# Kernel optimization log

Measured on AMD Instinct MI355X. Metric: run time of the kernel, lower is better.

The kernel has to match this reference:

```python
import jax, jax.numpy as jnp
import numpy as np

N, B, E, D, DQ, H = 20000, 32, 320000, 128, 1024, 2
L = N // B  # 625 nodes per graph (equal-size graphs -> static max_node_num)
NUM_GNN_LAYERS = 3


def setup_inputs() -> dict:
    key = jax.random.key(0)
    ks = jax.random.split(key, 32)
    rn = lambda k, s, scale=1.0: jax.random.normal(k, s, jnp.float32) * scale
    w = lambda k, fi, fo: rn(k, (fi, fo), 1.0 / np.sqrt(fi))
    inp = {
        'x': rn(ks[0], (N, D)),
        'edge_attr': rn(ks[1], (E, D)),
        'u': rn(ks[2], (B, D)),
        'qa_attr': rn(ks[3], (B, DQ)),
        # edge MLP: cat(src,dest,edge_attr,u[eb]) = 4D -> hidden D -> D
        'W_e1': w(ks[4], 4 * D, D), 'b_e1': jnp.zeros((D,)),
        'W_e2': w(ks[5], D, D), 'b_e2': jnp.zeros((D,)),
        # weight mlp: cat(edge_attr, u[eb]) = 2D -> 1 (num_layers=1)
        'W_w': w(ks[6], 2 * D, 1), 'b_w': jnp.zeros((1,)),
        # message mlp: cat(x[row], edge_attr) = 2D -> D -> D
        'W_m1': w(ks[7], 2 * D, D), 'b_m1': jnp.zeros((D,)),
        'W_m2': w(ks[8], D, D), 'b_m2': jnp.zeros((D,)),
        # update mlp: cat(x, received, u[nb]) = 3D -> D -> D
        'W_u1': w(ks[9], 3 * D, D), 'b_u1': jnp.zeros((D,)),
        'W_u2': w(ks[10], D, D), 'b_u2': jnp.zeros((D,)),
        # multihead att-pool: q from qa_attr (DQ) -> H*dk; k,v from evidence (D) -> H*dk
        'W_q': w(ks[11], DQ, D), 'b_q': jnp.zeros((D,)),
        'W_k': w(ks[12], D, D), 'b_k': jnp.zeros((D,)),
        'W_v': w(ks[13], D, D), 'b_v': jnp.zeros((D,)),
        'edge_index': jax.random.randint(ks[14], (2, E), 0, N, dtype=jnp.int32),
        'node_batch': (jnp.arange(N, dtype=jnp.int32) // L).astype(jnp.int32),
        'num_of_nodes': jnp.full((B,), L, dtype=jnp.int32),
    }
    return inp


def _mlp2(h, W1, b1, W2, b2):
    return jax.nn.relu(h @ W1 + b1) @ W2 + b2


def _seg_softmax(logits, seg, num):
    m = jax.ops.segment_max(logits, seg, num_segments=num)
    e = jnp.exp(logits - m[seg])
    s = jax.ops.segment_sum(e, seg, num_segments=num)
    return e / s[seg]


def reference(x, edge_attr, u, qa_attr,
              W_e1, b_e1, W_e2, b_e2, W_w, b_w,
              W_m1, b_m1, W_m2, b_m2, W_u1, b_u1, W_u2, b_u2,
              W_q, b_q, W_k, b_k, W_v, b_v,
              edge_index, node_batch, num_of_nodes):
    row, col = edge_index[0], edge_index[1]
    edge_batch = node_batch[row]
    Bsz, Nn = u.shape[0], x.shape[0]
    Lm = Nn // Bsz  # static max_node_num (equal-size graphs)

    norm_w = None
    for _ in range(NUM_GNN_LAYERS):
        ue = u[edge_batch]  # [E, D]
        # EdgeModel: cat(src, dest, edge_attr, u[eb]) -> MLP -> new edge_attr
        new_edge = _mlp2(jnp.concatenate([x[row], x[col], edge_attr, ue], 1),
                         W_e1, b_e1, W_e2, b_e2)
        # edge weights from OLD edge_attr (per EdgeV1Model.forward)
        wts = jnp.concatenate([edge_attr, ue], 1) @ W_w + b_w  # [E,1]
        norm_w = _seg_softmax(wts[:, 0], edge_batch, Bsz)[:, None]  # [E,1]
        edge_attr = new_edge
        # NodeModel: message MLP, weighted scatter_mean over col, update MLP
        msg = _mlp2(jnp.concatenate([x[row], edge_attr], 1), W_m1, b_m1, W_m2, b_m2)
        summed = jax.ops.segment_sum(msg * norm_w, col, num_segments=Nn)
        cnt = jax.ops.segment_sum(jnp.ones((msg.shape[0],), msg.dtype), col, num_segments=Nn)
        received = summed / jnp.maximum(cnt, 1.0)[:, None]
        x = _mlp2(jnp.concatenate([x, received, u[node_batch]], 1),
                  W_u1, b_u1, W_u2, b_u2)

    pooled_edge = jax.ops.segment_sum(edge_attr * norm_w, edge_batch, num_segments=Bsz)  # [B,D]
    # evidence packing: equal graphs -> simple reshape, then exact GELU
    evidence = jax.nn.gelu(x.reshape(Bsz, Lm, -1), approximate=False)  # [B,L,D]
    mask = jnp.arange(Lm)[None, :] >= num_of_nodes[:, None]  # [B,L] True = masked

    # MultiheadAttPoolLayer
    dk = W_k.shape[1] // H
    q = (qa_attr @ W_q + b_q).reshape(Bsz, H, dk)
    k = (evidence @ W_k + b_k).reshape(Bsz, Lm, H, dk)
    v = (evidence @ W_v + b_v).reshape(Bsz, Lm, H, dk)
    scores = jnp.einsum('bhd,blhd->bhl', q, k) / jnp.sqrt(jnp.float32(dk))
    scores = jnp.where(mask[:, None, :], -1e30, scores)
    attn = jax.nn.softmax(scores, axis=-1)
    pooled_node = jnp.einsum('bhl,blhd->bhd', attn, v).reshape(Bsz, H * dk)  # [B,D]

    return jnp.concatenate([pooled_edge, pooled_node], 1)  # [B, 2D]
```

## Files before the change

kernel.cpp:

```cpp
#include <hip/hip_runtime.h>
#include <math.h>

typedef __bf16 bf16_t;
typedef bf16_t bf16x8 __attribute__((ext_vector_type(8)));
typedef bf16_t bf16x4 __attribute__((ext_vector_type(4)));
typedef bf16_t bf16x2 __attribute__((ext_vector_type(2)));
typedef float  f32x4  __attribute__((ext_vector_type(4)));

#define N_NODES 20000
#define NEDGE   320000
#define DIM     128
#define TP      136
#define EBLK    2500
#define FBLK    10000
#define NBLK    625
#define GPRE    157
#define PBLK    512

#define FE1  0
#define FE2  49152
#define FM1  65536
#define FM2  98304
#define FU1  114688
#define FU2  163840
#define FK   180224
#define FV   196608
#define WF_ELEMS 212992

__device__ __forceinline__ void acc_zero32(f32x4 acc[2][8]) {
  f32x4 z = {0.f, 0.f, 0.f, 0.f};
#pragma unroll
  for (int i = 0; i < 2; ++i)
#pragma unroll
    for (int j = 0; j < 8; ++j) acc[i][j] = z;
}

__device__ __forceinline__ void wstage_rows_bf(bf16_t* sA, const bf16_t* src, int rowreg, int lane) {
  int r = lane >> 1, h = lane & 1;
  int row = __shfl(rowreg, r);
  const bf16_t* sp = src + (size_t)row * DIM + h * 64;
  bf16_t* dp = sA + r * TP + h * 64;
#pragma unroll
  for (int i = 0; i < 8; ++i)
    *(uint4*)(dp + i * 8) = *(const uint4*)(sp + i * 8);
}

__device__ __forceinline__ void wstage_rows_f32(bf16_t* sA, const float* src, int rowreg, int lane) {
  int r = lane >> 1, h = lane & 1;
  int row = __shfl(rowreg, r);
  const float* sp = src + (size_t)row * DIM + h * 64;
  bf16_t* dp = sA + r * TP + h * 64;
#pragma unroll
  for (int i = 0; i < 8; ++i) {
    float4 f0 = *(const float4*)(sp + i * 8);
    float4 f1 = *(const float4*)(sp + i * 8 + 4);
    bf16x8 tv;
    tv[0]=(bf16_t)f0.x; tv[1]=(bf16_t)f0.y; tv[2]=(bf16_t)f0.z; tv[3]=(bf16_t)f0.w;
    tv[4]=(bf16_t)f1.x; tv[5]=(bf16_t)f1.y; tv[6]=(bf16_t)f1.z; tv[7]=(bf16_t)f1.w;
    *(bf16x8*)(dp + i * 8) = tv;
  }
}

__device__ __forceinline__ void wstage_seq_bf(bf16_t* sA, const bf16_t* src, int base, int lane) {
  int r = lane >> 1, h = lane & 1;
  const bf16_t* sp = src + (size_t)(base + r) * DIM + h * 64;
  bf16_t* dp = sA + r * TP + h * 64;
#pragma unroll
  for (int i = 0; i < 8; ++i)
    *(uint4*)(dp + i * 8) = *(const uint4*)(sp + i * 8);
}

__device__ __forceinline__ void wstage_seq_f32(bf16_t* sA, const float* src, int base, int lane) {
  int r = lane >> 1, h = lane & 1;
  const float* sp = src + (size_t)(base + r) * DIM + h * 64;
  bf16_t* dp = sA + r * TP + h * 64;
#pragma unroll
  for (int i = 0; i < 8; ++i) {
    float4 f0 = *(const float4*)(sp + i * 8);
    float4 f1 = *(const float4*)(sp + i * 8 + 4);
    bf16x8 tv;
    tv[0]=(bf16_t)f0.x; tv[1]=(bf16_t)f0.y; tv[2]=(bf16_t)f0.z; tv[3]=(bf16_t)f0.w;
    tv[4]=(bf16_t)f1.x; tv[5]=(bf16_t)f1.y; tv[6]=(bf16_t)f1.z; tv[7]=(bf16_t)f1.w;
    *(bf16x8*)(dp + i * 8) = tv;
  }
}

__device__ __forceinline__ void chunk_stage(bf16_t* ch, const bf16_t* __restrict__ src, int t) {
#pragma unroll
  for (int i = 0; i < 8; ++i) {
    int idx = (i * 256 + t) * 8;
    *(uint4*)(ch + idx) = *(const uint4*)(src + idx);
  }
}

__device__ __forceinline__ void wmfma_lds(const bf16_t* sA, const bf16_t* ch,
                                          int lane, int lm, int lq, f32x4 acc[2][8]) {
#pragma unroll
  for (int kk = 0; kk < 4; ++kk) {
    int ko = kk * 32 + lq * 8;
    bf16x8 a0 = *(const bf16x8*)(sA + lm * TP + ko);
    bf16x8 a1 = *(const bf16x8*)(sA + (16 + lm) * TP + ko);
    const bf16_t* wp = ch + (kk << 12) + (lane << 3);
#pragma unroll
    for (int ct = 0; ct < 8; ++ct) {
      bf16x8 bfr = *(const bf16x8*)(wp + (ct << 9));
      acc[0][ct] = __builtin_amdgcn_mfma_f32_16x16x32_bf16(a0, bfr, acc[0][ct], 0, 0, 0);
      acc[1][ct] = __builtin_amdgcn_mfma_f32_16x16x32_bf16(a1, bfr, acc[1][ct], 0, 0, 0);
    }
  }
}

__device__ __forceinline__ void wmfma_gk128(const bf16_t* sA, const bf16_t* __restrict__ Wf,
                                            int lane, int lm, int lq, f32x4 acc[2][8]) {
#pragma unroll
  for (int kk = 0; kk < 4; ++kk) {
    int ko = kk * 32 + lq * 8;
    bf16x8 a0 = *(const bf16x8*)(sA + lm * TP + ko);
    bf16x8 a1 = *(const bf16x8*)(sA + (16 + lm) * TP + ko);
    const bf16_t* wp = Wf + ((kk * 8) << 9) + (lane << 3);
#pragma unroll
    for (int ct = 0; ct < 8; ++ct) {
      bf16x8 bfr = *(const bf16x8*)(wp + (ct << 9));
      acc[0][ct] = __builtin_amdgcn_mfma_f32_16x16x32_bf16(a0, bfr, acc[0][ct], 0, 0, 0);
      acc[1][ct] = __builtin_amdgcn_mfma_f32_16x16x32_bf16(a1, bfr, acc[1][ct], 0, 0, 0);
    }
  }
}

__device__ __forceinline__ void merge_shfl(float& m, float& s, int width) {
  for (int k = 1; k < width; k <<= 1) {
    float m2 = __shfl_xor(m, k), s2 = __shfl_xor(s, k);
    float M = fmaxf(m, m2), ns = 0.f;
    if (m  > -1e29f) ns += s  * expf(m  - M);
    if (m2 > -1e29f) ns += s2 * expf(m2 - M);
    m = M; s = ns;
  }
}

__global__ void gn_xcvt(const float* x, bf16_t* xb) {
  int i = blockIdx.x * 256 + threadIdx.x;
  if (i < N_NODES * DIM / 4) {
    float4 f = ((const float4*)x)[i];
    bf16x4 o; o[0]=(bf16_t)f.x; o[1]=(bf16_t)f.y; o[2]=(bf16_t)f.z; o[3]=(bf16_t)f.w;
    *(bf16x4*)(xb + (size_t)i * 4) = o;
  }
}

__global__ void gn_fragw(const float* We1, const float* We2, const float* Wm1, const float* Wm2,
                         const float* Wu1, const float* Wu2, const float* Wk, const float* Wv,
                         bf16_t* WF) {
  int idx = blockIdx.x * 256 + threadIdx.x;
  if (idx >= WF_ELEMS) return;
  int seg = idx >> 14;
  const float* W; int kc;
  switch (seg) {
    case 0:  W = We1; kc = 0; break;
    case 1:  W = We1; kc = 1; break;
    case 2:  W = We1; kc = 2; break;
    case 3:  W = We2; kc = 0; break;
    case 4:  W = Wm1; kc = 0; break;
    case 5:  W = Wm1; kc = 1; break;
    case 6:  W = Wm2; kc = 0; break;
    case 7:  W = Wu1; kc = 0; break;
    case 8:  W = Wu1; kc = 1; break;
    case 9:  W = Wu1; kc = 2; break;
    case 10: W = Wu2; kc = 0; break;
    case 11: W = Wk;  kc = 0; break;
    default: W = Wv;  kc = 0; break;
  }
  int r = idx & 16383;
  int j = r & 7, lane = (r >> 3) & 63, ct = (r >> 9) & 7, kk = (r >> 12) & 3;
  int k = kc * 128 + kk * 32 + (lane >> 4) * 8 + j;
  int n = ct * 16 + (lane & 15);
  WF[idx] = (bf16_t)W[k * 128 + n];
}

__global__ void gn_uprep(const float* u, const float* We1, const float* be1,
                         const float* Ww, const float* bw, float* Rp, float* uw) {
  int t = threadIdx.x;
  for (int idx = blockIdx.x * 256 + t; idx < 32 * 128; idx += gridDim.x * 256) {
    int g = idx >> 7, c = idx & 127;
    float acc = be1[c];
    for (int k = 0; k < 128; ++k) acc += u[g * 128 + k] * We1[(384 + k) * 128 + c];
    Rp[g * 128 + (c & 15) * 8 + (c >> 4)] = acc;
  }
  if (blockIdx.x == 0 && t < 32) {
    float acc = bw[0];
    for (int k = 0; k < 128; ++k) acc += u[t * 128 + k] * Ww[128 + k];
    uw[t] = acc;
  }
}

__global__ void gn_counti(const int* ei, int* cnti) {
  int e = blockIdx.x * 256 + threadIdx.x;
  if (e < NEDGE) atomicAdd(&cnti[ei[NEDGE + e]], 1);
}

__global__ void gn_scan(const int* cnti, int* off, int* curs) {
  __shared__ int part[256];
  int t = threadIdx.x;
  int base = t * 80;
  int lim = base + 80; if (lim > N_NODES) lim = N_NODES;
  int s = 0;
  for (int i = base; i < lim; ++i) s += cnti[i];
  part[t] = s;
  __syncthreads();
  for (int d = 1; d < 256; d <<= 1) {
    int add = (t >= d) ? part[t - d] : 0;
    __syncthreads();
    part[t] += add;
    __syncthreads();
  }
  int pfx = (t == 0) ? 0 : part[t - 1];
  for (int i = base; i < lim; ++i) {
    off[i] = pfx; curs[i] = pfx; pfx += cnti[i];
  }
  if (t == 0) off[N_NODES] = NEDGE;
}

__global__ void gn_eidx(const int* ei, int* curs, int* eidx) {
  int e = blockIdx.x * 256 + threadIdx.x;
  if (e < NEDGE) {
    int c = ei[NEDGE + e];
    int pos = atomicAdd(&curs[c], 1);
    eidx[pos] = e;
  }
}

__global__ void gn_q(const float* qa, const float* Wq, const float* bq, float* qb) {
  int b = blockIdx.x, t = threadIdx.x;
  int c = t & 127, half = t >> 7;
  const float* qrow = qa + b * 1024 + half * 512;
  float acc = 0.f;
  for (int k = 0; k < 512; ++k) acc += qrow[k] * Wq[(half * 512 + k) * 128 + c];
  __shared__ float red[256];
  red[t] = acc;
  __syncthreads();
  if (half == 0) qb[b * 128 + c] = red[c] + red[128 + c] + bq[c];
}

__global__ void gn_wl0(const float* ea, const float* Ww, const float* uw,
                       const int* ei, const int* nbat, float* wl, int* gb) {
  int t = threadIdx.x;
  int sub = t & 15, grp = t >> 4;
  for (int e = blockIdx.x * 16 + grp; e < NEDGE; e += gridDim.x * 16) {
    const float* er = ea + (size_t)e * DIM + sub * 8;
    float s = 0.f;
#pragma unroll
    for (int j = 0; j < 8; ++j) s += er[j] * Ww[sub * 8 + j];
#pragma unroll
    for (int m = 1; m < 16; m <<= 1) s += __shfl_xor(s, m);
    if (sub == 0) {
      int g = nbat[ei[e]];
      wl[e] = s + uw[g];
      gb[e] = g;
    }
  }
}

__global__ void gn_part0(const float* wl, const int* gb, float* pm, float* ps) {
  __shared__ float lv[128];
  __shared__ int   lgg[128];
  int t = threadIdx.x, blk = blockIdx.x, e0 = blk * 128;
  if (t < 128) { lv[t] = wl[e0 + t]; lgg[t] = gb[e0 + t]; }
  __syncthreads();
  int g = t >> 3, seg = t & 7;
  float m = -1e30f, s = 0.f;
  for (int i = seg * 16; i < seg * 16 + 16; ++i)
    if (lgg[i] == g) {
      float v = lv[i];
      if (v > m) { s = s * expf(m - v) + 1.f; m = v; }
      else s += expf(v - m);
    }
  merge_shfl(m, s, 8);
  if (seg == 0) { pm[blk * 32 + g] = m; ps[blk * 32 + g] = s; }
}

__global__ void gn_reduce_ms(const float* pm, const float* ps, float* mg, float* sg, int nb) {
  int g = blockIdx.x, t = threadIdx.x;
  __shared__ float red[256];
  float m = -1e30f;
  for (int i = t; i < nb; i += 256) m = fmaxf(m, pm[i * 32 + g]);
  red[t] = m; __syncthreads();
  for (int s2 = 128; s2 > 0; s2 >>= 1) { if (t < s2) red[t] = fmaxf(red[t], red[t + s2]); __syncthreads(); }
  m = red[0]; __syncthreads();
  float s = 0.f;
  for (int i = t; i < nb; i += 256) {
    float sb = ps[i * 32 + g];
    if (sb > 0.f) s += sb * expf(pm[i * 32 + g] - m);
  }
  red[t] = s; __syncthreads();
  for (int s2 = 128; s2 > 0; s2 >>= 1) { if (t < s2) red[t] += red[t + s2]; __syncthreads(); }
  if (t == 0) { mg[g] = m; sg[g] = red[0]; }
}

__global__ __launch_bounds__(256, 2) void gn_fused(
    const bf16_t* __restrict__ xb,
    const void* esrcv, int efirst,
    bf16_t* edst,
    const bf16_t* __restrict__ WF,
    const float* Rp, const float* UW, const float* Wwv,
    const float* be2, const float* bm1, const float* bm2,
    const float* wl_cur, const float* mg, const float* sg,
    float* wl_next, float* pm, float* ps, int last,
    const int* ei, const int* gb, bf16_t* msg,
    const float* uu, const float* bu1, const int* nbat, float* pre,
    float* nwout) {
  __shared__ bf16_t chunk[16384];
  __shared__ bf16_t band[4][32 * TP];
  __shared__ float slwt[128];

  int t = threadIdx.x;
  int w = t >> 6, lane = t & 63;
  int lm = lane & 15, lq = lane >> 4;
  int blk = blockIdx.x;
  bf16_t* myband = band[w];

  if (blk >= EBLK) {
    int nb128 = blk - EBLK;
    int gb32 = nb128 * 4 + w;
    int lrow = 0, lgr = 0;
    if (lane < 32) {
      int node = gb32 * 32 + lane;
      if (node > N_NODES - 1) node = N_NODES - 1;
      lrow = node;
      lgr = nbat[node];
    }
    f32x4 acc[2][8];
    acc_zero32(acc);
    wstage_rows_bf(myband, xb, lrow, lane);
    chunk_stage(chunk, WF + FU1, t);
    __syncthreads();
    wmfma_lds(myband, chunk, lane, lm, lq, acc);
    __syncthreads();
    wstage_rows_f32(myband, uu, lgr, lane);
    chunk_stage(chunk, WF + FU1 + 32768, t);
    __syncthreads();
    wmfma_lds(myband, chunk, lane, lm, lq, acc);
    if (gb32 < NBLK) {
      float* pp = pre + (size_t)gb32 * 4096 + lane;
#pragma unroll
      for (int rt = 0; rt < 2; ++rt)
#pragma unroll
        for (int reg = 0; reg < 4; ++reg)
#pragma unroll
          for (int ct = 0; ct < 8; ++ct)
            pp[((rt * 32 + reg * 8 + ct) << 6)] = acc[rt][ct][reg] + bu1[ct * 16 + lm];
    }
    return;
  }

  int e0 = blk * 128;
  int ew0 = e0 + w * 32;
  int lrowr = 0, lcolr = 0, lgr = 0;
  float lnwr = 0.f;
  if (lane < 32) {
    int e = ew0 + lane;
    lrowr = ei[e];
    lcolr = ei[NEDGE + e];
    lgr = gb[e];
    lnwr = expf(wl_cur[e] - mg[lgr]) / sg[lgr];
    if (last) nwout[e] = lnwr;
  }

  f32x4 accE[2][8], accM[2][8];
  acc_zero32(accE);
  acc_zero32(accM);

  uint4 c0, c1, c2, c3, c4, c5, c6, c7;
#define CLOAD(SRC) { const uint4* _s = (const uint4*)(SRC) + t; \
  c0 = _s[0];    c1 = _s[256];  c2 = _s[512];  c3 = _s[768]; \
  c4 = _s[1024]; c5 = _s[1280]; c6 = _s[1536]; c7 = _s[1792]; }
#define CWRITE() { uint4* _d = (uint4*)chunk + t; \
  _d[0] = c0;    _d[256] = c1;  _d[512] = c2;  _d[768] = c3; \
  _d[1024] = c4; _d[1280] = c5; _d[1536] = c6; _d[1792] = c7; }

  CLOAD(WF + FE1);
  wstage_rows_bf(myband, xb, lrowr, lane);
  CWRITE();
  __syncthreads();

  CLOAD(WF + FM1);
  wmfma_lds(myband, chunk, lane, lm, lq, accE);
  __syncthreads();
  CWRITE();
  __syncthreads();

  CLOAD(WF + FE1 + 16384);
  wmfma_lds(myband, chunk, lane, lm, lq, accM);
  wstage_rows_bf(myband, xb, lcolr, lane);
  __syncthreads();
  CWRITE();
  __syncthreads();

  CLOAD(WF + FE1 + 32768);
  wmfma_lds(myband, chunk, lane, lm, lq, accE);
  if (efirst) wstage_seq_f32(myband, (const float*)esrcv, ew0, lane);
  else        wstage_seq_bf (myband, (const bf16_t*)esrcv, ew0, lane);
  __syncthreads();
  CWRITE();
  __syncthreads();

  CLOAD(WF + FE2);
  wmfma_lds(myband, chunk, lane, lm, lq, accE);
#pragma unroll
  for (int rt = 0; rt < 2; ++rt)
#pragma unroll
    for (int reg = 0; reg < 4; ++reg) {
      int row = rt * 16 + lq * 4 + reg;
      int g = __shfl(lgr, row);
      const float4* rp = (const float4*)(Rp + (size_t)g * 128 + lm * 8);
      float4 ra = rp[0], rb = rp[1];
      float rv[8] = {ra.x, ra.y, ra.z, ra.w, rb.x, rb.y, rb.z, rb.w};
#pragma unroll
      for (int ct = 0; ct < 8; ++ct) {
        int col = ct * 16 + lm;
        myband[row * TP + col] = (bf16_t)fmaxf(accE[rt][ct][reg] + rv[ct], 0.f);
      }
    }
  acc_zero32(accE);
  __syncthreads();
  CWRITE();
  __syncthreads();

  CLOAD(WF + FM1 + 16384);
  wmfma_lds(myband, chunk, lane, lm, lq, accE);
  {
    float ww8[8], be8[8];
#pragma unroll
    for (int ct = 0; ct < 8; ++ct) { ww8[ct] = Wwv[ct * 16 + lm]; be8[ct] = be2[ct * 16 + lm]; }
#pragma unroll
    for (int rt = 0; rt < 2; ++rt)
#pragma unroll
      for (int reg = 0; reg < 4; ++reg) {
        int row = rt * 16 + lq * 4 + reg;
        int g = __shfl(lgr, row);
        float lsum = 0.f;
#pragma unroll
        for (int ct = 0; ct < 8; ++ct) {
          int col = ct * 16 + lm;
          float v = accE[rt][ct][reg] + be8[ct];
          myband[row * TP + col] = (bf16_t)v;
          lsum += v * ww8[ct];
        }
        if (!last) {
          lsum += __shfl_xor(lsum, 1);
          lsum += __shfl_xor(lsum, 2);
          lsum += __shfl_xor(lsum, 4);
          lsum += __shfl_xor(lsum, 8);
          if (lm == 0) {
            float v2 = lsum + UW[g];
            wl_next[ew0 + row] = v2;
            slwt[w * 32 + row] = v2;
          }
        }
      }
    int r = lane >> 1, h = lane & 1;
    bf16_t* dp = edst + (size_t)(ew0 + r) * DIM + h * 64;
    const bf16_t* sp2 = myband + r * TP + h * 64;
#pragma unroll
    for (int i = 0; i < 8; ++i)
      *(uint4*)(dp + i * 8) = *(const uint4*)(sp2 + i * 8);
  }
  __syncthreads();
  CWRITE();
  __syncthreads();

  CLOAD(WF + FM2);
  wmfma_lds(myband, chunk, lane, lm, lq, accM);
  {
    float bm18[8];
#pragma unroll
    for (int ct = 0; ct < 8; ++ct) bm18[ct] = bm1[ct * 16 + lm];
#pragma unroll
    for (int rt = 0; rt < 2; ++rt)
#pragma unroll
      for (int reg = 0; reg < 4; ++reg) {
        int row = rt * 16 + lq * 4 + reg;
#pragma unroll
        for (int ct = 0; ct < 8; ++ct) {
          int col = ct * 16 + lm;
          myband[row * TP + col] = (bf16_t)fmaxf(accM[rt][ct][reg] + bm18[ct], 0.f);
        }
      }
  }
  acc_zero32(accM);
  __syncthreads();
  CWRITE();
  __syncthreads();

  wmfma_lds(myband, chunk, lane, lm, lq, accM);
  {
    float bm28[8];
#pragma unroll
    for (int ct = 0; ct < 8; ++ct) bm28[ct] = bm2[ct * 16 + lm];
#pragma unroll
    for (int rt = 0; rt < 2; ++rt)
#pragma unroll
      for (int reg = 0; reg < 4; ++reg) {
        int row = rt * 16 + lq * 4 + reg;
        float nwv = __shfl(lnwr, row);
#pragma unroll
        for (int ct = 0; ct < 8; ++ct) {
          int col = ct * 16 + lm;
          myband[row * TP + col] = (bf16_t)((accM[rt][ct][reg] + bm28[ct]) * nwv);
        }
      }
    int r = lane >> 1, h = lane & 1;
    bf16_t* dp = msg + (size_t)(ew0 + r) * DIM + h * 64;
    const bf16_t* sp2 = myband + r * TP + h * 64;
#pragma unroll
    for (int i = 0; i < 8; ++i)
      *(uint4*)(dp + i * 8) = *(const uint4*)(sp2 + i * 8);
  }

  if (!last) {
    int g = lane >> 1, seg = lane & 1;
    float m = -1e30f, s = 0.f;
    for (int i = seg * 16; i < seg * 16 + 16; ++i) {
      int gi = __shfl(lgr, i);
      if (gi == g) {
        float v = slwt[w * 32 + i];
        if (v > m) { s = s * expf(m - v) + 1.f; m = v; }
        else s += expf(v - m);
      }
    }
    merge_shfl(m, s, 2);
    if (seg == 0) { pm[(blk * 4 + w) * 32 + g] = m; ps[(blk * 4 + w) * 32 + g] = s; }
  }
#undef CLOAD
#undef CWRITE
}

__global__ __launch_bounds__(256) void gn_gather(
    const bf16_t* __restrict__ msg, const int* __restrict__ off,
    const int* __restrict__ eidx, bf16_t* recvb) {
  int w = threadIdx.x >> 6, lane = threadIdx.x & 63;
  int n = blockIdx.x * 4 + w;
  int o0 = off[n], o1 = off[n + 1];
  float a0 = 0.f, a1 = 0.f;
  int i = o0;
  int e = (i < o1) ? eidx[i] : 0;
  for (; i < o1; ++i) {
    int en = (i + 1 < o1) ? eidx[i + 1] : 0;
    bf16x2 v = *(const bf16x2*)(msg + (size_t)e * DIM + lane * 2);
    a0 += (float)v[0];
    a1 += (float)v[1];
    e = en;
  }
  float ic = 1.f / fmaxf((float)(o1 - o0), 1.f);
  bf16x2 o; o[0] = (bf16_t)(a0 * ic); o[1] = (bf16_t)(a1 * ic);
  *(bf16x2*)(recvb + (size_t)n * DIM + lane * 2) = o;
}

__global__ __launch_bounds__(64, 3) void gn_node(
    bf16_t* xdst, const bf16_t* recvb, const float* pre,
    const bf16_t* __restrict__ WF, const float* bu2) {
  __shared__ bf16_t sA[32 * TP];

  int lane = threadIdx.x;
  int nb = blockIdx.x;
  int n0 = nb * 32;
  int lm = lane & 15, lq = lane >> 4;

  wstage_seq_bf(sA, recvb, n0, lane);

  f32x4 acc[2][8];
  acc_zero32(acc);
  wmfma_gk128(sA, WF + FU1 + 16384, lane, lm, lq, acc);

  const float* pp = pre + (size_t)nb * 4096 + lane;
#pragma unroll
  for (int rt = 0; rt < 2; ++rt)
#pragma unroll
    for (int reg = 0; reg < 4; ++reg) {
      int row = rt * 16 + lq * 4 + reg;
#pragma unroll
      for (int ct = 0; ct < 8; ++ct) {
        int col = ct * 16 + lm;
        sA[row * TP + col] = (bf16_t)fmaxf(acc[rt][ct][reg] + pp[((rt * 32 + reg * 8 + ct) << 6)], 0.f);
      }
    }
  acc_zero32(acc);
  wmfma_gk128(sA, WF + FU2, lane, lm, lq, acc);

  {
    float bu28[8];
#pragma unroll
    for (int ct = 0; ct < 8; ++ct) bu28[ct] = bu2[ct * 16 + lm];
#pragma unroll
    for (int rt = 0; rt < 2; ++rt)
#pragma unroll
      for (int reg = 0; reg < 4; ++reg) {
        int row = rt * 16 + lq * 4 + reg;
        bf16_t* dr = xdst + (size_t)(n0 + row) * DIM;
#pragma unroll
        for (int ct = 0; ct < 8; ++ct) {
          int col = ct * 16 + lm;
          dr[col] = (bf16_t)(acc[rt][ct][reg] + bu28[ct]);
        }
      }
  }
}

__global__ __launch_bounds__(64, 3) void gn_ev(
    const bf16_t* xsrc, const bf16_t* __restrict__ WF,
    const float* bk, const float* bv, float* kb, float* vb) {
  __shared__ bf16_t sA[32 * TP];

  int lane = threadIdx.x;
  int n0 = blockIdx.x * 32;
  int sel = blockIdx.y;
  const bf16_t* Wf = WF + (sel ? FV : FK);
  const float* bias = sel ? bv : bk;
  float* dst = sel ? vb : kb;
  int lm = lane & 15, lq = lane >> 4;

  {
    int r = lane >> 1, h = lane & 1;
    const bf16_t* sp = xsrc + (size_t)(n0 + r) * DIM + h * 64;
    bf16_t* dp = sA + r * TP + h * 64;
#pragma unroll
    for (int i = 0; i < 8; ++i) {
      uint4 v = *(const uint4*)(sp + i * 8);
      bf16_t tmp[8];
      *(uint4*)tmp = v;
      bf16x8 tv;
#pragma unroll
      for (int j = 0; j < 8; ++j) {
        float f = (float)tmp[j];
        tv[j] = (bf16_t)(0.5f * f * (1.f + erff(f * 0.70710678118654752f)));
      }
      *(bf16x8*)(dp + i * 8) = tv;
    }
  }

  f32x4 acc[2][8];
  acc_zero32(acc);
  wmfma_gk128(sA, Wf, lane, lm, lq, acc);

  {
    float b8[8];
#pragma unroll
    for (int ct = 0; ct < 8; ++ct) b8[ct] = bias[ct * 16 + lm];
#pragma unroll
    for (int rt = 0; rt < 2; ++rt)
#pragma unroll
      for (int reg = 0; reg < 4; ++reg) {
        int row = rt * 16 + lq * 4 + reg;
        float* dr = dst + (size_t)(n0 + row) * DIM;
#pragma unroll
        for (int ct = 0; ct < 8; ++ct) {
          int col = ct * 16 + lm;
          dr[col] = acc[rt][ct][reg] + b8[ct];
        }
      }
  }
}

__global__ __launch_bounds__(256, 2) void gn_pooled_edge(
    const bf16_t* __restrict__ eb, const float* __restrict__ nw,
    const int* __restrict__ gb, float* pep) {
  __shared__ float loc[4][4096];
  int t = threadIdx.x;
  int lane = t & 63, w = t >> 6;
  float* myloc = loc[w];
  for (int i = lane; i < 4096; i += 64) myloc[i] = 0.f;

  int wid = blockIdx.x * 4 + w;
  int c0 = lane * 2;
  for (int e = wid; e < NEDGE; e += PBLK * 4) {
    int g = gb[e];
    float nwt = nw[e];
    bf16x2 v = *(const bf16x2*)(eb + (size_t)e * DIM + c0);
    float* a = myloc + g * 128 + c0;
    float2 cur = *(float2*)a;
    cur.x += (float)v[0] * nwt;
    cur.y += (float)v[1] * nwt;
    *(float2*)a = cur;
  }
  __syncthreads();
  float* pp = pep + (size_t)blockIdx.x * 4096;
  for (int i = t; i < 4096; i += 256)
    pp[i] = loc[0][i] + loc[1][i] + loc[2][i] + loc[3][i];
}

__global__ void gn_att(const float* qb, const float* kb, const float* vb, const int* non, float* out) {
  int b = blockIdx.x >> 1, h = blockIdx.x & 1, t = threadIdx.x;
  __shared__ float qv[64];
  __shared__ float sc[625];
  __shared__ float red[256];
  if (t < 64) qv[t] = qb[b * 128 + h * 64 + t];
  __syncthreads();
  int nn = non[b];
  const float4* qv4 = (const float4*)qv;
  for (int l = t; l < 625; l += 256) {
    float acc = 0.f;
    const float4* kr = (const float4*)(kb + ((size_t)(b * 625 + l)) * DIM + h * 64);
#pragma unroll
    for (int d2 = 0; d2 < 16; ++d2) {
      float4 kv = kr[d2];
      float4 qq = qv4[d2];
      acc += qq.x * kv.x + qq.y * kv.y + qq.z * kv.z + qq.w * kv.w;
    }
    sc[l] = (l < nn) ? acc * 0.125f : -1e30f;
  }
  __syncthreads();
  float m = -1e30f;
  for (int l = t; l < 625; l += 256) m = fmaxf(m, sc[l]);
  red[t] = m; __syncthreads();
  for (int s2 = 128; s2 > 0; s2 >>= 1) { if (t < s2) red[t] = fmaxf(red[t], red[t + s2]); __syncthreads(); }
  m = red[0]; __syncthreads();
  float ssum = 0.f;
  for (int l = t; l < 625; l += 256) { float e = expf(sc[l] - m); sc[l] = e; ssum += e; }
  red[t] = ssum; __syncthreads();
  for (int s2 = 128; s2 > 0; s2 >>= 1) { if (t < s2) red[t] += red[t + s2]; __syncthreads(); }
  float inv = 1.f / red[0];
  __syncthreads();
  int d = t & 63, seg = t >> 6;
  float acc = 0.f;
  for (int l = seg; l < 625; l += 4) acc += sc[l] * vb[((size_t)(b * 625 + l)) * DIM + h * 64 + d];
  red[t] = acc; __syncthreads();
  if (t < 64) {
    float v = red[t] + red[64 + t] + red[128 + t] + red[192 + t];
    out[b * 256 + 128 + h * 64 + d] = v * inv;
  }
}

__global__ void gn_fin(const float* pep, float* out) {
  int i = blockIdx.x * 256 + threadIdx.x;
  float s = 0.f;
#pragma unroll 8
  for (int blk = 0; blk < PBLK; ++blk) s += pep[(size_t)blk * 4096 + i];
  int b = i >> 7, c = i & 127;
  out[b * 256 + c] = s;
}

extern "C" void kernel_launch(void* const* d_in, const int* in_sizes, int n_in,
                              void* d_out, int out_size, void* d_ws, size_t ws_size,
                              hipStream_t stream) {
  const float* x   = (const float*)d_in[0];
  const float* ea  = (const float*)d_in[1];
  const float* u   = (const float*)d_in[2];
  const float* qa  = (const float*)d_in[3];
  const float* We1 = (const float*)d_in[4];
  const float* be1 = (const float*)d_in[5];
  const float* We2 = (const float*)d_in[6];
  const float* be2 = (const float*)d_in[7];
  const float* Ww  = (const float*)d_in[8];
  const float* bw  = (const float*)d_in[9];
  const float* Wm1 = (const float*)d_in[10];
  const float* bm1 = (const float*)d_in[11];
  const float* Wm2 = (const float*)d_in[12];
  const float* bm2 = (const float*)d_in[13];
  const float* Wu1 = (const float*)d_in[14];
  const float* bu1 = (const float*)d_in[15];
  const float* Wu2 = (const float*)d_in[16];
  const float* bu2 = (const float*)d_in[17];
  const float* Wq  = (const float*)d_in[18];
  const float* bq  = (const float*)d_in[19];
  const float* Wk  = (const float*)d_in[20];
  const float* bk  = (const float*)d_in[21];
  const float* Wv  = (const float*)d_in[22];
  const float* bv  = (const float*)d_in[23];
  const int* ei   = (const int*)d_in[24];
  const int* nbat = (const int*)d_in[25];
  const int* non  = (const int*)d_in[26];
  float* out = (float*)d_out;

  char* p = (char*)d_ws;
  auto alloc = [&](size_t bytes) { char* r = p; p += (bytes + 255) & ~(size_t)255; return r; };
  bf16_t* EB    = (bf16_t*)alloc((size_t)NEDGE * DIM * 2);
  bf16_t* XB    = (bf16_t*)alloc((size_t)N_NODES * DIM * 2);
  bf16_t* XB0   = (bf16_t*)alloc((size_t)N_NODES * DIM * 2);
  bf16_t* MSG   = (bf16_t*)alloc((size_t)NEDGE * DIM * 2);
  bf16_t* RECVB = (bf16_t*)alloc((size_t)N_NODES * DIM * 2);
  int*   CNTI = (int*)alloc((size_t)N_NODES * 4);
  int*   OFF  = (int*)alloc((size_t)(N_NODES + 1) * 4);
  int*   CURS = (int*)alloc((size_t)N_NODES * 4);
  int*   EIDX = (int*)alloc((size_t)NEDGE * 4);
  float* WL   = (float*)alloc((size_t)NEDGE * 4);
  float* WLn  = (float*)alloc((size_t)NEDGE * 4);
  float* NW   = (float*)alloc((size_t)NEDGE * 4);
  int*   GB   = (int*)alloc((size_t)NEDGE * 4);
  float* PM   = (float*)alloc((size_t)FBLK * 32 * 4);
  float* PS   = (float*)alloc((size_t)FBLK * 32 * 4);
  float* MG   = (float*)alloc(32 * 4);
  float* SG   = (float*)alloc(32 * 4);
  float* RP   = (float*)alloc(32 * 128 * 4);
  float* UW   = (float*)alloc(32 * 4);
  bf16_t* WF  = (bf16_t*)alloc((size_t)WF_ELEMS * 2);
  float* QB   = (float*)alloc(32 * 128 * 4);
  float* KB   = (float*)alloc((size_t)N_NODES * DIM * 4);
  float* VB   = (float*)alloc((size_t)N_NODES * DIM * 4);
  float* PEP  = (float*)alloc((size_t)PBLK * 4096 * 4);
  float* PRE  = (float*)alloc((size_t)N_NODES * DIM * 4);

  hipMemsetAsync(CNTI, 0, (size_t)N_NODES * 4, stream);

  gn_xcvt<<<(N_NODES * DIM / 4 + 255) / 256, 256, 0, stream>>>(x, XB0);
  gn_fragw<<<(WF_ELEMS + 255) / 256, 256, 0, stream>>>(We1, We2, Wm1, Wm2, Wu1, Wu2, Wk, Wv, WF);
  gn_uprep<<<16, 256, 0, stream>>>(u, We1, be1, Ww, bw, RP, UW);
  gn_counti<<<1250, 256, 0, stream>>>(ei, CNTI);
  gn_scan<<<1, 256, 0, stream>>>(CNTI, OFF, CURS);
  gn_eidx<<<1250, 256, 0, stream>>>(ei, CURS, EIDX);
  gn_q<<<32, 256, 0, stream>>>(qa, Wq, bq, QB);
  gn_wl0<<<2500, 256, 0, stream>>>(ea, Ww, UW, ei, nbat, WL, GB);
  gn_part0<<<EBLK, 256, 0, stream>>>(WL, GB, PM, PS);

  for (int layer = 0; layer < 3; ++layer) {
    int first = (layer == 0) ? 1 : 0;
    int last = (layer == 2) ? 1 : 0;
    const bf16_t* xs = first ? XB0 : XB;
    const void* es = first ? (const void*)ea : (const void*)EB;
    float* cur = (layer == 1) ? WLn : WL;
    float* nxt = (layer == 1) ? WL : WLn;
    gn_reduce_ms<<<32, 256, 0, stream>>>(PM, PS, MG, SG, first ? EBLK : FBLK);
    gn_fused<<<EBLK + GPRE, 256, 0, stream>>>(xs, es, first, EB, WF, RP, UW, Ww,
                                              be2, bm1, bm2, cur, MG, SG,
                                              nxt, PM, PS, last, ei, GB, MSG,
                                              u, bu1, nbat, PRE, NW);
    gn_gather<<<5000, 256, 0, stream>>>(MSG, OFF, EIDX, RECVB);
    gn_node<<<NBLK, 64, 0, stream>>>(XB, RECVB, PRE, WF, bu2);
  }

  gn_pooled_edge<<<PBLK, 256, 0, stream>>>(EB, NW, GB, PEP);
  gn_ev<<<dim3(NBLK, 2), 64, 0, stream>>>(XB, WF, bk, bv, KB, VB);
  gn_att<<<64, 256, 0, stream>>>(QB, KB, VB, non, out);
  gn_fin<<<16, 256, 0, stream>>>(PEP, out);
}
```

Before: 1.334 ms.

## Fold message MLP second layer into update weights via precomputed Wm2·Wu1

Removes the second message-MLP GEMM from the per-edge fused kernel by using linearity. The mean aggregation commutes with the Wm2 projection, so the node kernel multiplies the aggregated hidden activations by a precomputed Wm2·Wu1 block and adds the bias term rnw·(bm2·Wu1). The gather kernel now also averages the per-edge normalized weights to rebuild that bias, and the per-block softmax partials are stored transposed for contiguous reduction reads. This removes one 128x128 GEMM per edge tile plus a weight chunk load, at the cost of always writing nwout and changing bf16 rounding points.

```diff
diff --git a/kernel.cpp b/kernel.cpp
--- a/kernel.cpp
+++ b/kernel.cpp
@@ -12,7 +12,7 @@
 #define DIM     128
 #define TP      136
 #define EBLK    2500
-#define FBLK    10000
+#define FWAVES  10000
 #define NBLK    625
 #define GPRE    157
 #define PBLK    512
@@ -25,7 +25,8 @@
 #define FU2  163840
 #define FK   180224
 #define FV   196608
-#define WF_ELEMS 212992
+#define FWC  212992
+#define WF_ELEMS 229376
 
 __device__ __forceinline__ void acc_zero32(f32x4 acc[2][8]) {
   f32x4 z = {0.f, 0.f, 0.f, 0.f};
@@ -146,9 +147,19 @@
   }
 }
 
+__global__ void gn_wcomb(const float* Wm2, const float* Wu1, float* wc) {
+  int idx = blockIdx.x * 256 + threadIdx.x;
+  if (idx >= 16384) return;
+  int i = idx >> 7, j = idx & 127;
+  float acc = 0.f;
+  for (int m = 0; m < 128; ++m)
+    acc += Wm2[i * 128 + m] * Wu1[(128 + m) * 128 + j];
+  wc[idx] = acc;
+}
+
 __global__ void gn_fragw(const float* We1, const float* We2, const float* Wm1, const float* Wm2,
                          const float* Wu1, const float* Wu2, const float* Wk, const float* Wv,
-                         bf16_t* WF) {
+                         const float* Wc, bf16_t* WF) {
   int idx = blockIdx.x * 256 + threadIdx.x;
   if (idx >= WF_ELEMS) return;
   int seg = idx >> 14;
@@ -166,7 +177,8 @@
     case 9:  W = Wu1; kc = 2; break;
     case 10: W = Wu2; kc = 0; break;
     case 11: W = Wk;  kc = 0; break;
-    default: W = Wv;  kc = 0; break;
+    case 12: W = Wv;  kc = 0; break;
+    default: W = Wc;  kc = 0; break;
   }
   int r = idx & 16383;
   int j = r & 7, lane = (r >> 3) & 63, ct = (r >> 9) & 7, kk = (r >> 12) & 3;
@@ -176,7 +188,9 @@
 }
 
 __global__ void gn_uprep(const float* u, const float* We1, const float* be1,
-                         const float* Ww, const float* bw, float* Rp, float* uw) {
+                         const float* Ww, const float* bw,
+                         const float* bm2, const float* Wu1,
+                         float* Rp, float* uw, float* bm2u) {
   int t = threadIdx.x;
   for (int idx = blockIdx.x * 256 + t; idx < 32 * 128; idx += gridDim.x * 256) {
     int g = idx >> 7, c = idx & 127;
@@ -188,6 +202,11 @@
     float acc = bw[0];
     for (int k = 0; k < 128; ++k) acc += u[t * 128 + k] * Ww[128 + k];
     uw[t] = acc;
+  }
+  if (blockIdx.x == 1 && t < 128) {
+    float acc = 0.f;
+    for (int k = 0; k < 128; ++k) acc += bm2[k] * Wu1[(128 + k) * 128 + t];
+    bm2u[t] = acc;
   }
 }
 
@@ -273,21 +292,21 @@
       else s += expf(v - m);
     }
   merge_shfl(m, s, 8);
-  if (seg == 0) { pm[blk * 32 + g] = m; ps[blk * 32 + g] = s; }
+  if (seg == 0) { pm[g * FWAVES + blk] = m; ps[g * FWAVES + blk] = s; }
 }
 
 __global__ void gn_reduce_ms(const float* pm, const float* ps, float* mg, float* sg, int nb) {
   int g = blockIdx.x, t = threadIdx.x;
   __shared__ float red[256];
   float m = -1e30f;
-  for (int i = t; i < nb; i += 256) m = fmaxf(m, pm[i * 32 + g]);
+  for (int i = t; i < nb; i += 256) m = fmaxf(m, pm[g * FWAVES + i]);
   red[t] = m; __syncthreads();
   for (int s2 = 128; s2 > 0; s2 >>= 1) { if (t < s2) red[t] = fmaxf(red[t], red[t + s2]); __syncthreads(); }
   m = red[0]; __syncthreads();
   float s = 0.f;
   for (int i = t; i < nb; i += 256) {
-    float sb = ps[i * 32 + g];
-    if (sb > 0.f) s += sb * expf(pm[i * 32 + g] - m);
+    float sb = ps[g * FWAVES + i];
+    if (sb > 0.f) s += sb * expf(pm[g * FWAVES + i] - m);
   }
   red[t] = s; __syncthreads();
   for (int s2 = 128; s2 > 0; s2 >>= 1) { if (t < s2) red[t] += red[t + s2]; __syncthreads(); }
@@ -300,7 +319,7 @@
     bf16_t* edst,
     const bf16_t* __restrict__ WF,
     const float* Rp, const float* UW, const float* Wwv,
-    const float* be2, const float* bm1, const float* bm2,
+    const float* be2, const float* bm1,
     const float* wl_cur, const float* mg, const float* sg,
     float* wl_next, float* pm, float* ps, int last,
     const int* ei, const int* gb, bf16_t* msg,
@@ -360,7 +379,7 @@
     lcolr = ei[NEDGE + e];
     lgr = gb[e];
     lnwr = expf(wl_cur[e] - mg[lgr]) / sg[lgr];
-    if (last) nwout[e] = lnwr;
+    nwout[e] = lnwr;
   }
 
   f32x4 accE[2][8], accM[2][8];
@@ -466,7 +485,6 @@
   CWRITE();
   __syncthreads();
 
-  CLOAD(WF + FM2);
   wmfma_lds(myband, chunk, lane, lm, lq, accM);
   {
     float bm18[8];
@@ -477,33 +495,11 @@
 #pragma unroll
       for (int reg = 0; reg < 4; ++reg) {
         int row = rt * 16 + lq * 4 + reg;
+        float nwv = __shfl(lnwr, row);
 #pragma unroll
         for (int ct = 0; ct < 8; ++ct) {
           int col = ct * 16 + lm;
-          myband[row * TP + col] = (bf16_t)fmaxf(accM[rt][ct][reg] + bm18[ct], 0.f);
-        }
-      }
-  }
-  acc_zero32(accM);
-  __syncthreads();
-  CWRITE();
-  __syncthreads();
-
-  wmfma_lds(myband, chunk, lane, lm, lq, accM);
-  {
-    float bm28[8];
-#pragma unroll
-    for (int ct = 0; ct < 8; ++ct) bm28[ct] = bm2[ct * 16 + lm];
-#pragma unroll
-    for (int rt = 0; rt < 2; ++rt)
-#pragma unroll
-      for (int reg = 0; reg < 4; ++reg) {
-        int row = rt * 16 + lq * 4 + reg;
-        float nwv = __shfl(lnwr, row);
-#pragma unroll
-        for (int ct = 0; ct < 8; ++ct) {
-          int col = ct * 16 + lm;
-          myband[row * TP + col] = (bf16_t)((accM[rt][ct][reg] + bm28[ct]) * nwv);
+          myband[row * TP + col] = (bf16_t)(fmaxf(accM[rt][ct][reg] + bm18[ct], 0.f) * nwv);
         }
       }
     int r = lane >> 1, h = lane & 1;
@@ -526,19 +522,20 @@
       }
     }
     merge_shfl(m, s, 2);
-    if (seg == 0) { pm[(blk * 4 + w) * 32 + g] = m; ps[(blk * 4 + w) * 32 + g] = s; }
+    if (seg == 0) { pm[g * FWAVES + blk * 4 + w] = m; ps[g * FWAVES + blk * 4 + w] = s; }
   }
 #undef CLOAD
 #undef CWRITE
 }
 
 __global__ __launch_bounds__(256) void gn_gather(
-    const bf16_t* __restrict__ msg, const int* __restrict__ off,
-    const int* __restrict__ eidx, bf16_t* recvb) {
+    const bf16_t* __restrict__ msg, const float* __restrict__ nw,
+    const int* __restrict__ off, const int* __restrict__ eidx,
+    bf16_t* recvb, float* rnw) {
   int w = threadIdx.x >> 6, lane = threadIdx.x & 63;
   int n = blockIdx.x * 4 + w;
   int o0 = off[n], o1 = off[n + 1];
-  float a0 = 0.f, a1 = 0.f;
+  float a0 = 0.f, a1 = 0.f, snw = 0.f;
   int i = o0;
   int e = (i < o1) ? eidx[i] : 0;
   for (; i < o1; ++i) {
@@ -546,16 +543,18 @@
     bf16x2 v = *(const bf16x2*)(msg + (size_t)e * DIM + lane * 2);
     a0 += (float)v[0];
     a1 += (float)v[1];
+    snw += nw[e];
     e = en;
   }
   float ic = 1.f / fmaxf((float)(o1 - o0), 1.f);
   bf16x2 o; o[0] = (bf16_t)(a0 * ic); o[1] = (bf16_t)(a1 * ic);
   *(bf16x2*)(recvb + (size_t)n * DIM + lane * 2) = o;
+  if (lane == 0) rnw[n] = snw * ic;
 }
 
 __global__ __launch_bounds__(64, 3) void gn_node(
-    bf16_t* xdst, const bf16_t* recvb, const float* pre,
-    const bf16_t* __restrict__ WF, const float* bu2) {
+    bf16_t* xdst, const bf16_t* recvb, const float* rnw, const float* pre,
+    const bf16_t* __restrict__ WF, const float* bu2, const float* bm2u) {
   __shared__ bf16_t sA[32 * TP];
 
   int lane = threadIdx.x;
@@ -563,22 +562,30 @@
   int n0 = nb * 32;
   int lm = lane & 15, lq = lane >> 4;
 
+  float rnwreg = 0.f;
+  if (lane < 32) rnwreg = rnw[n0 + lane];
+
   wstage_seq_bf(sA, recvb, n0, lane);
 
   f32x4 acc[2][8];
   acc_zero32(acc);
-  wmfma_gk128(sA, WF + FU1 + 16384, lane, lm, lq, acc);
+  wmfma_gk128(sA, WF + FWC, lane, lm, lq, acc);
 
   const float* pp = pre + (size_t)nb * 4096 + lane;
+  float bm2u8[8];
+#pragma unroll
+  for (int ct = 0; ct < 8; ++ct) bm2u8[ct] = bm2u[ct * 16 + lm];
 #pragma unroll
   for (int rt = 0; rt < 2; ++rt)
 #pragma unroll
     for (int reg = 0; reg < 4; ++reg) {
       int row = rt * 16 + lq * 4 + reg;
+      float rv = __shfl(rnwreg, row);
 #pragma unroll
       for (int ct = 0; ct < 8; ++ct) {
         int col = ct * 16 + lm;
-        sA[row * TP + col] = (bf16_t)fmaxf(acc[rt][ct][reg] + pp[((rt * 32 + reg * 8 + ct) << 6)], 0.f);
+        sA[row * TP + col] = (bf16_t)fmaxf(
+            acc[rt][ct][reg] + rv * bm2u8[ct] + pp[((rt * 32 + reg * 8 + ct) << 6)], 0.f);
       }
     }
   acc_zero32(acc);
@@ -782,13 +789,16 @@
   float* WL   = (float*)alloc((size_t)NEDGE * 4);
   float* WLn  = (float*)alloc((size_t)NEDGE * 4);
   float* NW   = (float*)alloc((size_t)NEDGE * 4);
+  float* RNW  = (float*)alloc((size_t)N_NODES * 4);
   int*   GB   = (int*)alloc((size_t)NEDGE * 4);
-  float* PM   = (float*)alloc((size_t)FBLK * 32 * 4);
-  float* PS   = (float*)alloc((size_t)FBLK * 32 * 4);
+  float* PM   = (float*)alloc((size_t)32 * FWAVES * 4);
+  float* PS   = (float*)alloc((size_t)32 * FWAVES * 4);
   float* MG   = (float*)alloc(32 * 4);
   float* SG   = (float*)alloc(32 * 4);
   float* RP   = (float*)alloc(32 * 128 * 4);
   float* UW   = (float*)alloc(32 * 4);
+  float* WCOMB= (float*)alloc(16384 * 4);
+  float* BM2U = (float*)alloc(128 * 4);
   bf16_t* WF  = (bf16_t*)alloc((size_t)WF_ELEMS * 2);
   float* QB   = (float*)alloc(32 * 128 * 4);
   float* KB   = (float*)alloc((size_t)N_NODES * DIM * 4);
@@ -799,8 +809,9 @@
   hipMemsetAsync(CNTI, 0, (size_t)N_NODES * 4, stream);
 
   gn_xcvt<<<(N_NODES * DIM / 4 + 255) / 256, 256, 0, stream>>>(x, XB0);
-  gn_fragw<<<(WF_ELEMS + 255) / 256, 256, 0, stream>>>(We1, We2, Wm1, Wm2, Wu1, Wu2, Wk, Wv, WF);
-  gn_uprep<<<16, 256, 0, stream>>>(u, We1, be1, Ww, bw, RP, UW);
+  gn_wcomb<<<64, 256, 0, stream>>>(Wm2, Wu1, WCOMB);
+  gn_fragw<<<(WF_ELEMS + 255) / 256, 256, 0, stream>>>(We1, We2, Wm1, Wm2, Wu1, Wu2, Wk, Wv, WCOMB, WF);
+  gn_uprep<<<16, 256, 0, stream>>>(u, We1, be1, Ww, bw, bm2, Wu1, RP, UW, BM2U);
   gn_counti<<<1250, 256, 0, stream>>>(ei, CNTI);
   gn_scan<<<1, 256, 0, stream>>>(CNTI, OFF, CURS);
   gn_eidx<<<1250, 256, 0, stream>>>(ei, CURS, EIDX);
@@ -815,13 +826,13 @@
     const void* es = first ? (const void*)ea : (const void*)EB;
     float* cur = (layer == 1) ? WLn : WL;
     float* nxt = (layer == 1) ? WL : WLn;
-    gn_reduce_ms<<<32, 256, 0, stream>>>(PM, PS, MG, SG, first ? EBLK : FBLK);
+    gn_reduce_ms<<<32, 256, 0, stream>>>(PM, PS, MG, SG, first ? EBLK : FWAVES);
     gn_fused<<<EBLK + GPRE, 256, 0, stream>>>(xs, es, first, EB, WF, RP, UW, Ww,
-                                              be2, bm1, bm2, cur, MG, SG,
+                                              be2, bm1, cur, MG, SG,
                                               nxt, PM, PS, last, ei, GB, MSG,
                                               u, bu1, nbat, PRE, NW);
-    gn_gather<<<5000, 256, 0, stream>>>(MSG, OFF, EIDX, RECVB);
-    gn_node<<<NBLK, 64, 0, stream>>>(XB, RECVB, PRE, WF, bu2);
+    gn_gather<<<5000, 256, 0, stream>>>(MSG, NW, OFF, EIDX, RECVB, RNW);
+    gn_node<<<NBLK, 64, 0, stream>>>(XB, RECVB, RNW, PRE, WF, bu2, BM2U);
   }
 
   gn_pooled_edge<<<PBLK, 256, 0, stream>>>(EB, NW, GB, PEP);
```

After: 1.320 ms. About the same (-1.0%).
